# Kernel tuning notes

Hardware: AMD Instinct MI355X
Metric: run time of the kernel (lower is better)

## Reference

```python
import jax, jax.numpy as jnp
import numpy as np

N_NODES = 100000
BN_EPS = 1e-5


def setup_inputs() -> dict:
    key = jax.random.key(0)
    ks = jax.random.split(key, 20)
    d, h, h2, nc = 128, 128, 64, 10
    E = 1_600_000
    x = jax.random.normal(ks[0], (N_NODES, d), jnp.float32)
    ei = jax.random.randint(ks[1], (2, E), 0, N_NODES, jnp.int64)
    s = 0.05
    return {
        "x": x,
        "ei": ei,
        "W1l": jax.random.normal(ks[2], (d, h), jnp.float32) * s,
        "b1l": jax.random.normal(ks[3], (h,), jnp.float32) * s,
        "W1r": jax.random.normal(ks[4], (d, h), jnp.float32) * s,
        "g1": jax.random.uniform(ks[5], (h,), jnp.float32) + 0.5,
        "be1": jax.random.normal(ks[6], (h,), jnp.float32) * s,
        "m1": jax.random.normal(ks[7], (h,), jnp.float32) * s,
        "v1": jax.random.uniform(ks[8], (h,), jnp.float32) + 0.5,
        "W2l": jax.random.normal(ks[9], (h, h2), jnp.float32) * s,
        "b2l": jax.random.normal(ks[10], (h2,), jnp.float32) * s,
        "W2r": jax.random.normal(ks[11], (h, h2), jnp.float32) * s,
        "g2": jax.random.uniform(ks[12], (h2,), jnp.float32) + 0.5,
        "be2": jax.random.normal(ks[13], (h2,), jnp.float32) * s,
        "m2": jax.random.normal(ks[14], (h2,), jnp.float32) * s,
        "v2": jax.random.uniform(ks[15], (h2,), jnp.float32) + 0.5,
        "Wh": jax.random.normal(ks[16], (h2, nc), jnp.float32) * s,
        "bh": jax.random.normal(ks[17], (nc,), jnp.float32) * s,
    }


def _sage_conv(x, src, dst, Wl, bl, Wr):
    # PyG SAGEConv: out_i = lin_l(mean_{j->i} x_j) + lin_r(x_i)
    msg = x[src]                                              # [E, d] gather
    agg = jax.ops.segment_sum(msg, dst, num_segments=N_NODES)
    cnt = jax.ops.segment_sum(jnp.ones_like(dst, x.dtype), dst, num_segments=N_NODES)
    agg = agg / jnp.maximum(cnt, 1.0)[:, None]                # mean aggregation
    return agg @ Wl + bl + x @ Wr


def _bn(x, g, b, m, v):
    # eval-mode BatchNorm1d with running stats
    return (x - m) * (g * jax.lax.rsqrt(v + BN_EPS)) + b


def reference(x, ei, W1l, b1l, W1r, g1, be1, m1, v1,
              W2l, b2l, W2r, g2, be2, m2, v2, Wh, bh):
    src, dst = ei[0], ei[1]
    h = jax.nn.relu(_bn(_sage_conv(x, src, dst, W1l, b1l, W1r), g1, be1, m1, v1))
    # dropout p=0.1 inactive in eval mode
    h = jax.nn.relu(_bn(_sage_conv(h, src, dst, W2l, b2l, W2r), g2, be2, m2, v2))
    return h @ Wh + bh
```

## Files before the change

kernel.cpp:

```cpp
#include <hip/hip_runtime.h>
#include <hip/hip_bf16.h>
#include <stdint.h>

#define N_NODES 100000
constexpr float BN_EPS = 1e-5f;

typedef __bf16 bf16x8 __attribute__((ext_vector_type(8)));
typedef float f32x4 __attribute__((ext_vector_type(4)));

__device__ inline unsigned int pk2(float a, float b) {
    __bf16 x = (__bf16)a, y = (__bf16)b;
    return (unsigned int)__builtin_bit_cast(unsigned short, x) |
           ((unsigned int)__builtin_bit_cast(unsigned short, y) << 16);
}

__global__ __launch_bounds__(256) void k_wbn(int wpB,
                                             const float* __restrict__ W1l,
                                             const float* __restrict__ W1r,
                                             const float* __restrict__ W2l,
                                             const float* __restrict__ W2r,
                                             __bf16* __restrict__ Wt1hi,
                                             __bf16* __restrict__ Wt1lo,
                                             __bf16* __restrict__ Wt2hi,
                                             __bf16* __restrict__ Wt2lo,
                                             const float* __restrict__ b1l,
                                             const float* __restrict__ g1,
                                             const float* __restrict__ be1,
                                             const float* __restrict__ m1,
                                             const float* __restrict__ v1,
                                             const float* __restrict__ b2l,
                                             const float* __restrict__ g2,
                                             const float* __restrict__ be2,
                                             const float* __restrict__ m2,
                                             const float* __restrict__ v2,
                                             float* __restrict__ bn) {
    if ((int)blockIdx.x < wpB) {
        int idx = blockIdx.x * 256 + threadIdx.x;
        const float* W; __bf16 *Whi, *Wlo; int halfN, lidx;
        if (idx < 2 * 128 * 128) {
            lidx = idx; halfN = 128; Whi = Wt1hi; Wlo = Wt1lo;
            W = ((lidx >> 7) < 128) ? W1l : W1r;
        } else {
            lidx = idx - 2 * 128 * 128;
            if (lidx >= 2 * 64 * 128) return;
            halfN = 64; Whi = Wt2hi; Wlo = Wt2lo;
            W = ((lidx >> 7) < 64) ? W2l : W2r;
        }
        int c = lidx >> 7, k = lidx & 127;
        int cc = (c < halfN) ? c : c - halfN;
        float v = W[(size_t)k * halfN + cc];
        __bf16 h = (__bf16)v;
        Whi[lidx] = h;
        Wlo[lidx] = (__bf16)(v - (float)h);
        return;
    }
    int t = threadIdx.x;
    if (t < 128) {
        float S = g1[t] * rsqrtf(v1[t] + BN_EPS);
        bn[t] = S;
        bn[128 + t] = (b1l[t] - m1[t]) * S + be1[t];
    } else if (t < 192) {
        int f = t - 128;
        float S = g2[f] * rsqrtf(v2[f] + BN_EPS);
        bn[256 + f] = S;
        bn[320 + f] = (b2l[f] - m2[f]) * S + be2[f];
    }
}

template <int SPLITC>
__device__ void mfma_body(const float* __restrict__ A,
                          const __bf16* __restrict__ Wthi,
                          const __bf16* __restrict__ Wtlo,
                          __bf16* __restrict__ Cl, float* __restrict__ Cr,
                          int M, int bid) {
    constexpr int K = 128;
    __shared__ __bf16 sB[2][128][40];
    const int tid = threadIdx.x;
    const int lane = tid & 63;
    const int wave = tid >> 6;
    const int row0 = bid * 128 + wave * 32;
    const int rlo = lane & 15;
    const int rhi = lane >> 4;

    const int sc = tid >> 1;
    const int sseg = (tid & 1) * 16;

    f32x4 acc[4][2][2] = {};

    for (int k0 = 0; k0 < K; k0 += 32) {
        if (k0) __syncthreads();
        {
            const __bf16* gh = Wthi + (size_t)sc * K + k0 + sseg;
            const __bf16* gl = Wtlo + (size_t)sc * K + k0 + sseg;
            *(bf16x8*)(&sB[0][sc][sseg])     = *(const bf16x8*)gh;
            *(bf16x8*)(&sB[0][sc][sseg + 8]) = *(const bf16x8*)(gh + 8);
            *(bf16x8*)(&sB[1][sc][sseg])     = *(const bf16x8*)gl;
            *(bf16x8*)(&sB[1][sc][sseg + 8]) = *(const bf16x8*)(gl + 8);
        }
        bf16x8 ahi[2], alo[2];
        #pragma unroll
        for (int wr = 0; wr < 2; ++wr) {
            int row = row0 + wr * 16 + rlo;
            row = row < M ? row : M - 1;
            const float* ap = A + (size_t)row * K + k0 + rhi * 8;
            float4 v0 = *(const float4*)ap;
            float4 v1 = *(const float4*)(ap + 4);
            float vv[8] = {v0.x, v0.y, v0.z, v0.w, v1.x, v1.y, v1.z, v1.w};
            #pragma unroll
            for (int i = 0; i < 8; ++i) {
                __bf16 h = (__bf16)vv[i];
                ahi[wr][i] = h;
                alo[wr][i] = (__bf16)(vv[i] - (float)h);
            }
        }
        __syncthreads();
        #pragma unroll
        for (int cs = 0; cs < 4; ++cs) {
            #pragma unroll
            for (int cf = 0; cf < 2; ++cf) {
                int c = cs * 32 + cf * 16 + rlo;
                bf16x8 bhi = *(const bf16x8*)(&sB[0][c][rhi * 8]);
                bf16x8 blo = *(const bf16x8*)(&sB[1][c][rhi * 8]);
                #pragma unroll
                for (int wr = 0; wr < 2; ++wr) {
                    f32x4 a = acc[cs][wr][cf];
                    a = __builtin_amdgcn_mfma_f32_16x16x32_bf16(ahi[wr], bhi, a, 0, 0, 0);
                    a = __builtin_amdgcn_mfma_f32_16x16x32_bf16(ahi[wr], blo, a, 0, 0, 0);
                    a = __builtin_amdgcn_mfma_f32_16x16x32_bf16(alo[wr], bhi, a, 0, 0, 0);
                    acc[cs][wr][cf] = a;
                }
            }
        }
    }

    #pragma unroll
    for (int cs = 0; cs < 4; ++cs)
        #pragma unroll
        for (int cf = 0; cf < 2; ++cf) {
            int c = cs * 32 + cf * 16 + rlo;
            #pragma unroll
            for (int wr = 0; wr < 2; ++wr)
                #pragma unroll
                for (int r = 0; r < 4; ++r) {
                    int row = row0 + wr * 16 + rhi * 4 + r;
                    if (row < M) {
                        float val = acc[cs][wr][cf][r];
                        if (c < SPLITC)
                            Cl[(size_t)row * SPLITC + c] = (__bf16)val;
                        else
                            Cr[(size_t)row * (128 - SPLITC) + (c - SPLITC)] = val;
                    }
                }
        }
}

__global__ __launch_bounds__(256) void k_prep_gemm(const unsigned int* __restrict__ w,
                                                   int E, int* __restrict__ idx32,
                                                   int* __restrict__ rank,
                                                   int* __restrict__ deg,
                                                   int prepB, int chunk,
                                                   const float* __restrict__ A,
                                                   const __bf16* __restrict__ Wthi,
                                                   const __bf16* __restrict__ Wtlo,
                                                   __bf16* __restrict__ Cl, int M) {
    int bid = blockIdx.x;
    if (bid < prepB) {
        unsigned int wv = w[1 + 2 * (threadIdx.x & 63)];
        int f = __any(wv != 0);
        int lo = bid * chunk;
        int hi = min(lo + chunk, E);
        for (int e = lo + (int)threadIdx.x; e < hi; e += 256) {
            int s = (int)(f ? w[e] : w[2 * (size_t)e]);
            int d = (int)(f ? w[E + e] : w[2 * ((size_t)E + e)]);
            idx32[e] = s;
            idx32[E + e] = d;
            rank[e] = atomicAdd(&deg[d], 1);
        }
        return;
    }
    mfma_body<128>(A, Wthi, Wtlo, Cl, nullptr, M, bid - prepB);
}

__global__ __launch_bounds__(256) void k_scan1(const int* __restrict__ deg,
                                               int* __restrict__ offs,
                                               int* __restrict__ bsum, int n) {
    __shared__ int s[256];
    int t = threadIdx.x;
    int i = blockIdx.x * 256 + t;
    int v = (i < n) ? deg[i] : 0;
    s[t] = v;
    __syncthreads();
    for (int off = 1; off < 256; off <<= 1) {
        int add = (t >= off) ? s[t - off] : 0;
        __syncthreads();
        s[t] += add;
        __syncthreads();
    }
    if (i < n) offs[i] = s[t] - v;
    if (t == 255) bsum[blockIdx.x] = s[255];
}

__global__ __launch_bounds__(256) void k_scan2(int* __restrict__ bsum, int nb) {
    __shared__ int s[256];
    __shared__ int carry;
    int t = threadIdx.x;
    if (t == 0) carry = 0;
    __syncthreads();
    for (int base = 0; base < nb; base += 256) {
        int i = base + t;
        int v = (i < nb) ? bsum[i] : 0;
        s[t] = v;
        __syncthreads();
        for (int off = 1; off < 256; off <<= 1) {
            int add = (t >= off) ? s[t - off] : 0;
            __syncthreads();
            s[t] += add;
            __syncthreads();
        }
        if (i < nb) bsum[i] = s[t] - v + carry;
        __syncthreads();
        if (t == 0) carry += s[255];
        __syncthreads();
    }
}

__global__ void k_scan3(int* __restrict__ offs, const int* __restrict__ bsum,
                        int n, int E) {
    int i = blockIdx.x * blockDim.x + threadIdx.x;
    if (i < n) offs[i] += bsum[i >> 8];
    if (i == 0) offs[n] = E;
}

__global__ __launch_bounds__(256) void k_gemm_scat(const float* __restrict__ A,
                                                   const __bf16* __restrict__ Wthi,
                                                   const __bf16* __restrict__ Wtlo,
                                                   float* __restrict__ Cr, int M,
                                                   int G,
                                                   const int* __restrict__ idx32,
                                                   const int* __restrict__ rank,
                                                   const int* __restrict__ offs,
                                                   int* __restrict__ csr, int E) {
    int bid = blockIdx.x;
    if (bid < G) {
        mfma_body<0>(A, Wthi, Wtlo, nullptr, Cr, M, bid);
        return;
    }
    bid -= G;
    int base = bid * 1024 + threadIdx.x;
    #pragma unroll
    for (int k = 0; k < 4; ++k) {
        int e = base + k * 256;
        if (e < E) {
            int d = idx32[E + e];
            csr[offs[d] + rank[e]] = idx32[e];
        }
    }
}

__global__ __launch_bounds__(256) void k_mfma2(const __bf16* __restrict__ A,
                                               const __bf16* __restrict__ Wthi,
                                               const __bf16* __restrict__ Wtlo,
                                               __bf16* __restrict__ Cl,
                                               float* __restrict__ Cr, int M) {
    constexpr int K = 128;
    constexpr int SPLITC = 64;
    __shared__ __bf16 sB[2][128][40];
    const int tid = threadIdx.x;
    const int lane = tid & 63;
    const int wave = tid >> 6;
    const int row0 = blockIdx.x * 128 + wave * 32;
    const int rlo = lane & 15;
    const int rhi = lane >> 4;
    const int sc = tid >> 1;
    const int sseg = (tid & 1) * 16;

    f32x4 acc[4][2][2] = {};

    for (int k0 = 0; k0 < K; k0 += 32) {
        if (k0) __syncthreads();
        {
            const __bf16* gh = Wthi + (size_t)sc * K + k0 + sseg;
            const __bf16* gl = Wtlo + (size_t)sc * K + k0 + sseg;
            *(bf16x8*)(&sB[0][sc][sseg])     = *(const bf16x8*)gh;
            *(bf16x8*)(&sB[0][sc][sseg + 8]) = *(const bf16x8*)(gh + 8);
            *(bf16x8*)(&sB[1][sc][sseg])     = *(const bf16x8*)gl;
            *(bf16x8*)(&sB[1][sc][sseg + 8]) = *(const bf16x8*)(gl + 8);
        }
        bf16x8 a[2];
        #pragma unroll
        for (int wr = 0; wr < 2; ++wr) {
            int row = row0 + wr * 16 + rlo;
            row = row < M ? row : M - 1;
            a[wr] = *(const bf16x8*)(A + (size_t)row * K + k0 + rhi * 8);
        }
        __syncthreads();
        #pragma unroll
        for (int cs = 0; cs < 4; ++cs) {
            #pragma unroll
            for (int cf = 0; cf < 2; ++cf) {
                int c = cs * 32 + cf * 16 + rlo;
                bf16x8 bhi = *(const bf16x8*)(&sB[0][c][rhi * 8]);
                bf16x8 blo = *(const bf16x8*)(&sB[1][c][rhi * 8]);
                #pragma unroll
                for (int wr = 0; wr < 2; ++wr) {
                    f32x4 v = acc[cs][wr][cf];
                    v = __builtin_amdgcn_mfma_f32_16x16x32_bf16(a[wr], bhi, v, 0, 0, 0);
                    v = __builtin_amdgcn_mfma_f32_16x16x32_bf16(a[wr], blo, v, 0, 0, 0);
                    acc[cs][wr][cf] = v;
                }
            }
        }
    }

    #pragma unroll
    for (int cs = 0; cs < 4; ++cs)
        #pragma unroll
        for (int cf = 0; cf < 2; ++cf) {
            int c = cs * 32 + cf * 16 + rlo;
            #pragma unroll
            for (int wr = 0; wr < 2; ++wr)
                #pragma unroll
                for (int r = 0; r < 4; ++r) {
                    int row = row0 + wr * 16 + rhi * 4 + r;
                    if (row < M) {
                        float val = acc[cs][wr][cf][r];
                        if (c < SPLITC)
                            Cl[(size_t)row * SPLITC + c] = (__bf16)val;
                        else
                            Cr[(size_t)row * (128 - SPLITC) + (c - SPLITC)] = val;
                    }
                }
        }
}

template <int LOGF>
__global__ __launch_bounds__(256) void k_agg(const __bf16* __restrict__ xl,
                                             const float* __restrict__ lin,
                                             const int* __restrict__ csr,
                                             const int* __restrict__ offs,
                                             const float* __restrict__ S,
                                             const float* __restrict__ T,
                                             void* __restrict__ out, int N) {
    constexpr int F = 1 << LOGF;
    constexpr int NW = (F == 128) ? 8 : 4;
    int node = blockIdx.x * 4 + (threadIdx.x >> 6);
    if (node >= N) return;
    int lane = threadIdx.x & 63;
    int sub = lane >> 4;
    int col = lane & 15;
    int beg = offs[node], end = offs[node + 1];
    float inv = 1.0f / fmaxf((float)(end - beg), 1.0f);

    float sx[NW];
    #pragma unroll
    for (int j = 0; j < NW; ++j) sx[j] = 0.f;

    int e = beg;
    while (e < end) {
        int bl = min(64, end - e);
        int myidx = (lane < bl) ? csr[e + lane] : 0;
        int u = 0;
        for (; u + 8 <= bl; u += 8) {
            int s0 = __shfl(myidx, u + sub, 64);
            int s1 = __shfl(myidx, u + 4 + sub, 64);
            if constexpr (F == 128) {
                uint4 t0 = *(const uint4*)((const char*)xl + (size_t)s0 * 256 + col * 16);
                uint4 t1 = *(const uint4*)((const char*)xl + (size_t)s1 * 256 + col * 16);
                unsigned int w0[4] = {t0.x, t0.y, t0.z, t0.w};
                unsigned int w1[4] = {t1.x, t1.y, t1.z, t1.w};
                #pragma unroll
                for (int i = 0; i < 4; ++i) {
                    sx[2 * i]     += __uint_as_float(w0[i] << 16) + __uint_as_float(w1[i] << 16);
                    sx[2 * i + 1] += __uint_as_float(w0[i] & 0xffff0000u) + __uint_as_float(w1[i] & 0xffff0000u);
                }
            } else {
                uint2 t0 = *(const uint2*)((const char*)xl + (size_t)s0 * 128 + col * 8);
                uint2 t1 = *(const uint2*)((const char*)xl + (size_t)s1 * 128 + col * 8);
                unsigned int w0[2] = {t0.x, t0.y};
                unsigned int w1[2] = {t1.x, t1.y};
                #pragma unroll
                for (int i = 0; i < 2; ++i) {
                    sx[2 * i]     += __uint_as_float(w0[i] << 16) + __uint_as_float(w1[i] << 16);
                    sx[2 * i + 1] += __uint_as_float(w0[i] & 0xffff0000u) + __uint_as_float(w1[i] & 0xffff0000u);
                }
            }
        }
        for (; u + 4 <= bl; u += 4) {
            int s0 = __shfl(myidx, u + sub, 64);
            if constexpr (F == 128) {
                uint4 t0 = *(const uint4*)((const char*)xl + (size_t)s0 * 256 + col * 16);
                unsigned int w0[4] = {t0.x, t0.y, t0.z, t0.w};
                #pragma unroll
                for (int i = 0; i < 4; ++i) {
                    sx[2 * i]     += __uint_as_float(w0[i] << 16);
                    sx[2 * i + 1] += __uint_as_float(w0[i] & 0xffff0000u);
                }
            } else {
                uint2 t0 = *(const uint2*)((const char*)xl + (size_t)s0 * 128 + col * 8);
                unsigned int w0[2] = {t0.x, t0.y};
                #pragma unroll
                for (int i = 0; i < 2; ++i) {
                    sx[2 * i]     += __uint_as_float(w0[i] << 16);
                    sx[2 * i + 1] += __uint_as_float(w0[i] & 0xffff0000u);
                }
            }
        }
        if (u < bl) {
            int rr = u + sub;
            int s0 = __shfl(myidx, rr < bl ? rr : u, 64);
            bool ok = rr < bl;
            if constexpr (F == 128) {
                uint4 t0 = *(const uint4*)((const char*)xl + (size_t)s0 * 256 + col * 16);
                unsigned int w0[4] = {t0.x, t0.y, t0.z, t0.w};
                #pragma unroll
                for (int i = 0; i < 4; ++i) {
                    sx[2 * i]     += ok ? __uint_as_float(w0[i] << 16) : 0.f;
                    sx[2 * i + 1] += ok ? __uint_as_float(w0[i] & 0xffff0000u) : 0.f;
                }
            } else {
                uint2 t0 = *(const uint2*)((const char*)xl + (size_t)s0 * 128 + col * 8);
                unsigned int w0[2] = {t0.x, t0.y};
                #pragma unroll
                for (int i = 0; i < 2; ++i) {
                    sx[2 * i]     += ok ? __uint_as_float(w0[i] << 16) : 0.f;
                    sx[2 * i + 1] += ok ? __uint_as_float(w0[i] & 0xffff0000u) : 0.f;
                }
            }
        }
        e += bl;
    }

    #pragma unroll
    for (int j = 0; j < NW; ++j) {
        sx[j] += __shfl_xor(sx[j], 16, 64);
        sx[j] += __shfl_xor(sx[j], 32, 64);
    }

    if (sub == 0) {
        if constexpr (F == 128) {
            const float4* lp = (const float4*)(lin + (size_t)node * 128 + col * 8);
            float4 l0 = lp[0], l1 = lp[1];
            const float4* Sp = (const float4*)(S + col * 8);
            const float4* Tp = (const float4*)(T + col * 8);
            float4 Sa = Sp[0], Sb = Sp[1], Ta = Tp[0], Tb = Tp[1];
            float lv[8] = {l0.x, l0.y, l0.z, l0.w, l1.x, l1.y, l1.z, l1.w};
            float Sv[8] = {Sa.x, Sa.y, Sa.z, Sa.w, Sb.x, Sb.y, Sb.z, Sb.w};
            float Tv[8] = {Ta.x, Ta.y, Ta.z, Ta.w, Tb.x, Tb.y, Tb.z, Tb.w};
            unsigned int u[4];
            #pragma unroll
            for (int i = 0; i < 4; ++i) {
                float y0 = fmaxf(fmaf(fmaf(sx[2 * i], inv, lv[2 * i]), Sv[2 * i], Tv[2 * i]), 0.f);
                float y1 = fmaxf(fmaf(fmaf(sx[2 * i + 1], inv, lv[2 * i + 1]), Sv[2 * i + 1], Tv[2 * i + 1]), 0.f);
                u[i] = pk2(y0, y1);
            }
            *(uint4*)((char*)out + (size_t)node * 256 + col * 16) = make_uint4(u[0], u[1], u[2], u[3]);
        } else {
            float4 l = *(const float4*)(lin + (size_t)node * 64 + col * 4);
            float4 Sv = *(const float4*)(S + col * 4);
            float4 Tv = *(const float4*)(T + col * 4);
            float4 o;
            o.x = fmaxf(fmaf(fmaf(sx[0], inv, l.x), Sv.x, Tv.x), 0.f);
            o.y = fmaxf(fmaf(fmaf(sx[1], inv, l.y), Sv.y, Tv.y), 0.f);
            o.z = fmaxf(fmaf(fmaf(sx[2], inv, l.z), Sv.z, Tv.z), 0.f);
            o.w = fmaxf(fmaf(fmaf(sx[3], inv, l.w), Sv.w, Tv.w), 0.f);
            *(float4*)((float*)out + (size_t)node * 64 + col * 4) = o;
        }
    }
}

__global__ __launch_bounds__(256) void k_head(const float* __restrict__ h2,
                                              const float* __restrict__ Wh,
                                              const float* __restrict__ bh,
                                              float* __restrict__ out, int M) {
    __shared__ float sW[64 * 10];
    __shared__ float sb[10];
    for (int i = threadIdx.x; i < 640; i += 256) sW[i] = Wh[i];
    if (threadIdx.x < 10) sb[threadIdx.x] = bh[threadIdx.x];
    __syncthreads();
    int n = blockIdx.x * blockDim.x + threadIdx.x;
    if (n >= M) return;
    float acc[10];
    #pragma unroll
    for (int c = 0; c < 10; ++c) acc[c] = sb[c];
    const float* hr = h2 + (size_t)n * 64;
    #pragma unroll
    for (int k = 0; k < 64; ++k) {
        float hv = hr[k];
        #pragma unroll
        for (int c = 0; c < 10; ++c) acc[c] = fmaf(hv, sW[k * 10 + c], acc[c]);
    }
    #pragma unroll
    for (int c = 0; c < 10; ++c) out[(size_t)n * 10 + c] = acc[c];
}

static inline size_t align256(size_t x) { return (x + 255) & ~(size_t)255; }

extern "C" void kernel_launch(void* const* d_in, const int* in_sizes, int n_in,
                              void* d_out, int out_size, void* d_ws, size_t ws_size,
                              hipStream_t stream) {
    const float* x   = (const float*)d_in[0];
    const void*  ei  = d_in[1];
    const float* W1l = (const float*)d_in[2];
    const float* b1l = (const float*)d_in[3];
    const float* W1r = (const float*)d_in[4];
    const float* g1  = (const float*)d_in[5];
    const float* be1 = (const float*)d_in[6];
    const float* m1  = (const float*)d_in[7];
    const float* v1  = (const float*)d_in[8];
    const float* W2l = (const float*)d_in[9];
    const float* b2l = (const float*)d_in[10];
    const float* W2r = (const float*)d_in[11];
    const float* g2  = (const float*)d_in[12];
    const float* be2 = (const float*)d_in[13];
    const float* m2  = (const float*)d_in[14];
    const float* v2  = (const float*)d_in[15];
    const float* Wh  = (const float*)d_in[16];
    const float* bh  = (const float*)d_in[17];
    float* out = (float*)d_out;

    const int N = N_NODES;
    const int E = in_sizes[1] / 2;
    const int NB = (N + 255) / 256;

    char* p = (char*)d_ws;
    int* idx32 = (int*)p;  p += align256((size_t)2 * E * 4);
    int* rank  = (int*)p;  p += align256((size_t)E * 4);
    int* csr   = (int*)p;  p += align256((size_t)E * 4);
    int* offs  = (int*)p;  p += align256((size_t)(N + 1) * 4);
    int* deg   = (int*)p;  p += align256((size_t)N * 4);
    int* bsum  = (int*)p;  p += 4096;
    float* bn  = (float*)p; p += 4096;
    __bf16* Wt1hi = (__bf16*)p; p += align256((size_t)256 * 128 * 2);
    __bf16* Wt1lo = (__bf16*)p; p += align256((size_t)256 * 128 * 2);
    __bf16* Wt2hi = (__bf16*)p; p += align256((size_t)128 * 128 * 2);
    __bf16* Wt2lo = (__bf16*)p; p += align256((size_t)128 * 128 * 2);
    __bf16* xl = (__bf16*)p; p += align256((size_t)N * 128 * 2);
    float* xr  = (float*)p;  p += (size_t)N * 128 * 4;
    __bf16* hb = (__bf16*)p; p += align256((size_t)N * 128 * 2);
    __bf16* t2l = xl;
    float* t2r  = xr;
    float* h2   = (float*)hb;

    dim3 blk(256);
    const int WPB = (2 * 128 * 128 + 2 * 64 * 128 + 255) / 256;
    int G = (N + 127) / 128;
    int binBlocks = (E + 1023) / 1024;
    const int prepB = 512;
    int chunk = (E + prepB - 1) / prepB;

    hipMemsetAsync(deg, 0, (size_t)N * 4, stream);
    k_wbn<<<dim3(WPB + 1), blk, 0, stream>>>(WPB,
        W1l, W1r, W2l, W2r, Wt1hi, Wt1lo, Wt2hi, Wt2lo,
        b1l, g1, be1, m1, v1, b2l, g2, be2, m2, v2, bn);

    k_prep_gemm<<<dim3(prepB + G), blk, 0, stream>>>(
        (const unsigned int*)ei, E, idx32, rank, deg, prepB, chunk,
        x, Wt1hi, Wt1lo, xl, N);

    k_scan1<<<dim3(NB), blk, 0, stream>>>(deg, offs, bsum, N);
    k_scan2<<<dim3(1), blk, 0, stream>>>(bsum, NB);
    k_scan3<<<dim3(NB), blk, 0, stream>>>(offs, bsum, N, E);

    k_gemm_scat<<<dim3(G + binBlocks), blk, 0, stream>>>(
        x, Wt1hi + 128 * 128, Wt1lo + 128 * 128, xr, N, G,
        idx32, rank, offs, csr, E);

    k_agg<7><<<dim3((N + 3) / 4), blk, 0, stream>>>(
        xl, xr, csr, offs, bn, bn + 128, hb, N);

    k_mfma2<<<dim3(G), blk, 0, stream>>>(hb, Wt2hi, Wt2lo, t2l, t2r, N);
    k_agg<6><<<dim3((N + 3) / 4), blk, 0, stream>>>(
        t2l, t2r, csr, offs, bn + 256, bn + 320, h2, N);

    k_head<<<dim3((N + 255) / 256), blk, 0, stream>>>(h2, Wh, bh, out, N);
}
```

Measured before the change: 279.9 us.

## Use single-pass decoupled lookback scan, packed edge pairs, and bf16 root-linear outputs

```diff
diff --git a/kernel.cpp b/kernel.cpp
--- a/kernel.cpp
+++ b/kernel.cpp
@@ -155,7 +155,7 @@
 }
 
 __global__ __launch_bounds__(256) void k_prep_gemm(const unsigned int* __restrict__ w,
-                                                   int E, int* __restrict__ idx32,
+                                                   int E, int2* __restrict__ idx2,
                                                    int* __restrict__ rank,
                                                    int* __restrict__ deg,
                                                    int prepB, int chunk,
@@ -172,8 +172,7 @@
         for (int e = lo + (int)threadIdx.x; e < hi; e += 256) {
             int s = (int)(f ? w[e] : w[2 * (size_t)e]);
             int d = (int)(f ? w[E + e] : w[2 * ((size_t)E + e)]);
-            idx32[e] = s;
-            idx32[E + e] = d;
+            idx2[e] = make_int2(s, d);
             rank[e] = atomicAdd(&deg[d], 1);
         }
         return;
@@ -181,12 +180,17 @@
     mfma_body<128>(A, Wthi, Wtlo, Cl, nullptr, M, bid - prepB);
 }
 
-__global__ __launch_bounds__(256) void k_scan1(const int* __restrict__ deg,
-                                               int* __restrict__ offs,
-                                               int* __restrict__ bsum, int n) {
+__global__ __launch_bounds__(256) void k_scan_lb(const int* __restrict__ deg,
+                                                 int* __restrict__ offs,
+                                                 int* __restrict__ flagA,
+                                                 int* __restrict__ aggA,
+                                                 int* __restrict__ prefA,
+                                                 int n, int E) {
     __shared__ int s[256];
+    __shared__ int blockExcl;
     int t = threadIdx.x;
-    int i = blockIdx.x * 256 + t;
+    int b = blockIdx.x;
+    int i = b * 256 + t;
     int v = (i < n) ? deg[i] : 0;
     s[t] = v;
     __syncthreads();
@@ -196,53 +200,49 @@
         s[t] += add;
         __syncthreads();
     }
-    if (i < n) offs[i] = s[t] - v;
-    if (t == 255) bsum[blockIdx.x] = s[255];
-}
-
-__global__ __launch_bounds__(256) void k_scan2(int* __restrict__ bsum, int nb) {
-    __shared__ int s[256];
-    __shared__ int carry;
-    int t = threadIdx.x;
-    if (t == 0) carry = 0;
+    int total = s[255];
+    if (t == 0) {
+        if (b == 0) {
+            prefA[0] = total;
+            __hip_atomic_store(&flagA[0], 2, __ATOMIC_RELEASE, __HIP_MEMORY_SCOPE_AGENT);
+            blockExcl = 0;
+        } else {
+            __hip_atomic_store(&aggA[b], total, __ATOMIC_RELAXED, __HIP_MEMORY_SCOPE_AGENT);
+            __hip_atomic_store(&flagA[b], 1, __ATOMIC_RELEASE, __HIP_MEMORY_SCOPE_AGENT);
+            int running = 0;
+            int j = b - 1;
+            while (true) {
+                int f = __hip_atomic_load(&flagA[j], __ATOMIC_ACQUIRE, __HIP_MEMORY_SCOPE_AGENT);
+                if (f == 0) continue;
+                if (f == 2) {
+                    running += __hip_atomic_load(&prefA[j], __ATOMIC_RELAXED, __HIP_MEMORY_SCOPE_AGENT);
+                    break;
+                }
+                running += __hip_atomic_load(&aggA[j], __ATOMIC_RELAXED, __HIP_MEMORY_SCOPE_AGENT);
+                --j;
+            }
+            prefA[b] = running + total;
+            __hip_atomic_store(&flagA[b], 2, __ATOMIC_RELEASE, __HIP_MEMORY_SCOPE_AGENT);
+            blockExcl = running;
+        }
+    }
     __syncthreads();
-    for (int base = 0; base < nb; base += 256) {
-        int i = base + t;
-        int v = (i < nb) ? bsum[i] : 0;
-        s[t] = v;
-        __syncthreads();
-        for (int off = 1; off < 256; off <<= 1) {
-            int add = (t >= off) ? s[t - off] : 0;
-            __syncthreads();
-            s[t] += add;
-            __syncthreads();
-        }
-        if (i < nb) bsum[i] = s[t] - v + carry;
-        __syncthreads();
-        if (t == 0) carry += s[255];
-        __syncthreads();
-    }
-}
-
-__global__ void k_scan3(int* __restrict__ offs, const int* __restrict__ bsum,
-                        int n, int E) {
-    int i = blockIdx.x * blockDim.x + threadIdx.x;
-    if (i < n) offs[i] += bsum[i >> 8];
+    if (i < n) offs[i] = blockExcl + s[t] - v;
     if (i == 0) offs[n] = E;
 }
 
 __global__ __launch_bounds__(256) void k_gemm_scat(const float* __restrict__ A,
                                                    const __bf16* __restrict__ Wthi,
                                                    const __bf16* __restrict__ Wtlo,
-                                                   float* __restrict__ Cr, int M,
+                                                   __bf16* __restrict__ Cl, int M,
                                                    int G,
-                                                   const int* __restrict__ idx32,
+                                                   const int2* __restrict__ idx2,
                                                    const int* __restrict__ rank,
                                                    const int* __restrict__ offs,
                                                    int* __restrict__ csr, int E) {
     int bid = blockIdx.x;
     if (bid < G) {
-        mfma_body<0>(A, Wthi, Wtlo, nullptr, Cr, M, bid);
+        mfma_body<128>(A, Wthi, Wtlo, Cl, nullptr, M, bid);
         return;
     }
     bid -= G;
@@ -251,8 +251,8 @@
     for (int k = 0; k < 4; ++k) {
         int e = base + k * 256;
         if (e < E) {
-            int d = idx32[E + e];
-            csr[offs[d] + rank[e]] = idx32[e];
+            int2 sd = idx2[e];
+            csr[offs[sd.y] + rank[e]] = sd.x;
         }
     }
 }
@@ -261,7 +261,7 @@
                                                const __bf16* __restrict__ Wthi,
                                                const __bf16* __restrict__ Wtlo,
                                                __bf16* __restrict__ Cl,
-                                               float* __restrict__ Cr, int M) {
+                                               __bf16* __restrict__ Cr, int M) {
     constexpr int K = 128;
     constexpr int SPLITC = 64;
     __shared__ __bf16 sB[2][128][40];
@@ -327,7 +327,7 @@
                         if (c < SPLITC)
                             Cl[(size_t)row * SPLITC + c] = (__bf16)val;
                         else
-                            Cr[(size_t)row * (128 - SPLITC) + (c - SPLITC)] = val;
+                            Cr[(size_t)row * (128 - SPLITC) + (c - SPLITC)] = (__bf16)val;
                     }
                 }
         }
@@ -335,7 +335,7 @@
 
 template <int LOGF>
 __global__ __launch_bounds__(256) void k_agg(const __bf16* __restrict__ xl,
-                                             const float* __restrict__ lin,
+                                             const __bf16* __restrict__ lin,
                                              const int* __restrict__ csr,
                                              const int* __restrict__ offs,
                                              const float* __restrict__ S,
@@ -438,12 +438,17 @@
 
     if (sub == 0) {
         if constexpr (F == 128) {
-            const float4* lp = (const float4*)(lin + (size_t)node * 128 + col * 8);
-            float4 l0 = lp[0], l1 = lp[1];
+            uint4 l4 = *(const uint4*)((const char*)lin + ((size_t)node * 128 + col * 8) * 2);
+            unsigned int lw[4] = {l4.x, l4.y, l4.z, l4.w};
+            float lv[8];
+            #pragma unroll
+            for (int i = 0; i < 4; ++i) {
+                lv[2 * i]     = __uint_as_float(lw[i] << 16);
+                lv[2 * i + 1] = __uint_as_float(lw[i] & 0xffff0000u);
+            }
             const float4* Sp = (const float4*)(S + col * 8);
             const float4* Tp = (const float4*)(T + col * 8);
             float4 Sa = Sp[0], Sb = Sp[1], Ta = Tp[0], Tb = Tp[1];
-            float lv[8] = {l0.x, l0.y, l0.z, l0.w, l1.x, l1.y, l1.z, l1.w};
             float Sv[8] = {Sa.x, Sa.y, Sa.z, Sa.w, Sb.x, Sb.y, Sb.z, Sb.w};
             float Tv[8] = {Ta.x, Ta.y, Ta.z, Ta.w, Tb.x, Tb.y, Tb.z, Tb.w};
             unsigned int u[4];
@@ -455,14 +460,16 @@
             }
             *(uint4*)((char*)out + (size_t)node * 256 + col * 16) = make_uint4(u[0], u[1], u[2], u[3]);
         } else {
-            float4 l = *(const float4*)(lin + (size_t)node * 64 + col * 4);
+            uint2 l2 = *(const uint2*)((const char*)lin + ((size_t)node * 64 + col * 4) * 2);
+            float lv[4] = {__uint_as_float(l2.x << 16), __uint_as_float(l2.x & 0xffff0000u),
+                           __uint_as_float(l2.y << 16), __uint_as_float(l2.y & 0xffff0000u)};
             float4 Sv = *(const float4*)(S + col * 4);
             float4 Tv = *(const float4*)(T + col * 4);
             float4 o;
-            o.x = fmaxf(fmaf(fmaf(sx[0], inv, l.x), Sv.x, Tv.x), 0.f);
-            o.y = fmaxf(fmaf(fmaf(sx[1], inv, l.y), Sv.y, Tv.y), 0.f);
-            o.z = fmaxf(fmaf(fmaf(sx[2], inv, l.z), Sv.z, Tv.z), 0.f);
-            o.w = fmaxf(fmaf(fmaf(sx[3], inv, l.w), Sv.w, Tv.w), 0.f);
+            o.x = fmaxf(fmaf(fmaf(sx[0], inv, lv[0]), Sv.x, Tv.x), 0.f);
+            o.y = fmaxf(fmaf(fmaf(sx[1], inv, lv[1]), Sv.y, Tv.y), 0.f);
+            o.z = fmaxf(fmaf(fmaf(sx[2], inv, lv[2]), Sv.z, Tv.z), 0.f);
+            o.w = fmaxf(fmaf(fmaf(sx[3], inv, lv[3]), Sv.w, Tv.w), 0.f);
             *(float4*)((float*)out + (size_t)node * 64 + col * 4) = o;
         }
     }
@@ -523,22 +530,24 @@
     const int NB = (N + 255) / 256;
 
     char* p = (char*)d_ws;
-    int* idx32 = (int*)p;  p += align256((size_t)2 * E * 4);
+    int2* idx2 = (int2*)p; p += align256((size_t)E * 8);
     int* rank  = (int*)p;  p += align256((size_t)E * 4);
     int* csr   = (int*)p;  p += align256((size_t)E * 4);
     int* offs  = (int*)p;  p += align256((size_t)(N + 1) * 4);
     int* deg   = (int*)p;  p += align256((size_t)N * 4);
-    int* bsum  = (int*)p;  p += 4096;
+    int* flagA = (int*)p;  p += align256((size_t)NB * 4);
+    int* aggA  = (int*)p;  p += align256((size_t)NB * 4);
+    int* prefA = (int*)p;  p += align256((size_t)NB * 4);
     float* bn  = (float*)p; p += 4096;
     __bf16* Wt1hi = (__bf16*)p; p += align256((size_t)256 * 128 * 2);
     __bf16* Wt1lo = (__bf16*)p; p += align256((size_t)256 * 128 * 2);
     __bf16* Wt2hi = (__bf16*)p; p += align256((size_t)128 * 128 * 2);
     __bf16* Wt2lo = (__bf16*)p; p += align256((size_t)128 * 128 * 2);
     __bf16* xl = (__bf16*)p; p += align256((size_t)N * 128 * 2);
-    float* xr  = (float*)p;  p += (size_t)N * 128 * 4;
+    __bf16* xr = (__bf16*)p; p += align256((size_t)N * 128 * 2);
     __bf16* hb = (__bf16*)p; p += align256((size_t)N * 128 * 2);
     __bf16* t2l = xl;
-    float* t2r  = xr;
+    __bf16* t2r = xr;
     float* h2   = (float*)hb;
 
     dim3 blk(256);
@@ -548,22 +557,20 @@
     const int prepB = 512;
     int chunk = (E + prepB - 1) / prepB;
 
-    hipMemsetAsync(deg, 0, (size_t)N * 4, stream);
+    hipMemsetAsync(deg, 0, align256((size_t)N * 4) + (size_t)NB * 4, stream);
     k_wbn<<<dim3(WPB + 1), blk, 0, stream>>>(WPB,
         W1l, W1r, W2l, W2r, Wt1hi, Wt1lo, Wt2hi, Wt2lo,
         b1l, g1, be1, m1, v1, b2l, g2, be2, m2, v2, bn);
 
     k_prep_gemm<<<dim3(prepB + G), blk, 0, stream>>>(
-        (const unsigned int*)ei, E, idx32, rank, deg, prepB, chunk,
+        (const unsigned int*)ei, E, idx2, rank, deg, prepB, chunk,
         x, Wt1hi, Wt1lo, xl, N);
 
-    k_scan1<<<dim3(NB), blk, 0, stream>>>(deg, offs, bsum, N);
-    k_scan2<<<dim3(1), blk, 0, stream>>>(bsum, NB);
-    k_scan3<<<dim3(NB), blk, 0, stream>>>(offs, bsum, N, E);
+    k_scan_lb<<<dim3(NB), blk, 0, stream>>>(deg, offs, flagA, aggA, prefA, N, E);
 
     k_gemm_scat<<<dim3(G + binBlocks), blk, 0, stream>>>(
         x, Wt1hi + 128 * 128, Wt1lo + 128 * 128, xr, N, G,
-        idx32, rank, offs, csr, E);
+        idx2, rank, offs, csr, E);
 
     k_agg<7><<<dim3((N + 3) / 4), blk, 0, stream>>>(
         xl, xr, csr, offs, bn, bn + 128, hb, N);
```

Result: slower. 396.6 us (+41.7%).
